# Performance work log

Measured on AMD Instinct MI355X. Metric: run time of the kernel, lower is better.

## Reference

```python
import jax, jax.numpy as jnp
import numpy as np

EPS = 1e-12  # F.normalize eps


def setup_inputs() -> dict:
    key = jax.random.key(0)
    k1, k2 = jax.random.split(key)
    B, T, C, E = 4, 4096, 2048, 64
    return {
        "hidden_states": jax.random.normal(k1, (B, T, C), dtype=jnp.float32),
        "sim_matrix": jax.random.normal(k2, (C, E), dtype=jnp.float32),
        "gates": jnp.zeros((E,), dtype=jnp.float32),
        "min_experts": 2,
    }


def reference(hidden_states, sim_matrix, gates, min_experts):
    b, t, c = hidden_states.shape
    h = hidden_states.reshape(b * t, c)
    # L2-normalize tokens (dim=-1) and expert columns (dim=0)
    hn = h / jnp.maximum(jnp.linalg.norm(h, axis=-1, keepdims=True), EPS)
    wn = sim_matrix / jnp.maximum(jnp.linalg.norm(sim_matrix, axis=0, keepdims=True), EPS)
    logits = hn @ wn - jax.nn.sigmoid(gates)          # [N, E]
    gated = jax.nn.relu(logits)
    # STE threshold (forward: hard 0/1 indicator)
    ind = (gated > 0).astype(gated.dtype)
    mask = gated + jax.lax.stop_gradient(ind - gated)
    # fallback: rows with no active expert get top-min_experts of raw logits
    inactive = jnp.sum(ind, axis=1) == 0              # [N]
    _, topk_idx = jax.lax.top_k(logits, min_experts)  # [N, k]
    n = mask.shape[0]
    fallback = jnp.zeros((n, logits.shape[1]), dtype=bool).at[
        jnp.arange(n)[:, None], topk_idx].set(True)
    put = inactive[:, None] & fallback                # positions overwritten with 1.0
    mask = jnp.where(put, jnp.asarray(1.0, mask.dtype), mask)
    masked = jnp.where(mask > 0, gated, -jnp.inf)
    routing_weights = jax.nn.softmax(masked, axis=-1)
    return routing_weights, logits, mask
```

## Files before the change

### kernel.cpp

```cpp
#include <hip/hip_runtime.h>
#include <math.h>

#define CDIM 2048
#define EDIM 64
#define BM   32
#define WSEG 512
#define NITW 8
#define PREPB 8

#define SCALE_H 1024.0f
#define SCALE_W 4096.0f
#define INV_SCALE (1.0f / 4194304.0f)

typedef float    f32x16 __attribute__((ext_vector_type(16)));
typedef float    f32x4v __attribute__((ext_vector_type(4)));
typedef _Float16 f16x8  __attribute__((ext_vector_type(8)));
typedef __fp16   cvt_t  __attribute__((ext_vector_type(2)));

__global__ void prep_w(const float* __restrict__ W,
                       unsigned short* __restrict__ bfrag,
                       float* __restrict__ pnw) {
    __shared__ float tile[256][65];
    __shared__ float part[4][64];
    const int t = threadIdx.x;
    const int c0 = blockIdx.x * 256;
#pragma unroll
    for (int p = 0; p < 16; ++p) {
        int r = (t >> 4) + p * 16;
        float4 v = *reinterpret_cast<const float4*>(W + (size_t)(c0 + r) * EDIM + (t & 15) * 4);
        tile[r][(t & 15) * 4 + 0] = v.x;
        tile[r][(t & 15) * 4 + 1] = v.y;
        tile[r][(t & 15) * 4 + 2] = v.z;
        tile[r][(t & 15) * 4 + 3] = v.w;
    }
    __syncthreads();
    {
        int g = t >> 6, e = t & 63;
        float s = 0.f;
#pragma unroll
        for (int j = 0; j < 64; ++j) { float v = tile[g * 64 + j][e]; s += v * v; }
        part[g][e] = s;
    }
    __syncthreads();
    if (t < 64) pnw[blockIdx.x * EDIM + t] = part[0][t] + part[1][t] + part[2][t] + part[3][t];

    const int nt = t >> 7, hl = (t >> 6) & 1, lane = t & 63;
    const int e = nt * 32 + (lane & 31);
    const int kb = (lane >> 5) * 8;
#pragma unroll
    for (int s = 0; s < 16; ++s) {
        int kl = s * 16 + kb;
        unsigned int wds[4];
#pragma unroll
        for (int pj = 0; pj < 4; ++pj) {
            float v0 = tile[kl + 2 * pj][e] * SCALE_W;
            float v1 = tile[kl + 2 * pj + 1][e] * SCALE_W;
            cvt_t hh = __builtin_amdgcn_cvt_pkrtz(v0, v1);
            if (hl) {
                cvt_t ll = __builtin_amdgcn_cvt_pkrtz(v0 - (float)hh[0], v1 - (float)hh[1]);
                wds[pj] = __builtin_bit_cast(unsigned int, ll);
            } else {
                wds[pj] = __builtin_bit_cast(unsigned int, hh);
            }
        }
        size_t off = ((size_t)(blockIdx.x * 16 + s)) * 2048 + (size_t)nt * 1024 + (size_t)hl * 512 + (size_t)lane * 8;
        *reinterpret_cast<uint4*>(bfrag + off) = make_uint4(wds[0], wds[1], wds[2], wds[3]);
    }
}

__launch_bounds__(256, 2)
__global__ void gating_main(const float* __restrict__ H,
                            const unsigned short* __restrict__ bfrag,
                            const float* __restrict__ pnw,
                            const float* __restrict__ gates,
                            float* __restrict__ out_rw,
                            float* __restrict__ out_lg,
                            float* __restrict__ out_mk) {
    __shared__ float aS[4][32][64];
    __shared__ float red[4][32][68];
    __shared__ float normred[4][32];
    __shared__ float invw_s[64];
    __shared__ float sig_s[64];

    const int t = threadIdx.x;
    const int w = t >> 6;
    const int l = t & 63;
    const int row0 = blockIdx.x * BM;
    const int kg = l >> 5;
    const int arow = l & 31;
    const int srow4 = l >> 4;
    const int sch = l & 15;

    if (t < 64) {
        float s2 = 0.f;
#pragma unroll
        for (int b = 0; b < PREPB; ++b) s2 += pnw[b * EDIM + t];
        invw_s[t] = 1.f / fmaxf(sqrtf(s2), 1e-12f);
        sig_s[t] = 1.f / (1.f + __expf(-gates[t]));
    }

    f32x16 acc[2][3];
#pragma unroll
    for (int a = 0; a < 2; ++a)
#pragma unroll
        for (int b = 0; b < 3; ++b)
#pragma unroll
            for (int i = 0; i < 16; ++i) acc[a][b][i] = 0.f;
    float nacc = 0.f;

#define STAGE1(J, IT) { \
    const int row_ = 4 * (J) + srow4; \
    const float* src_ = H + (size_t)(row0 + row_) * CDIM + w * WSEG + (IT) * 64 + ((sch ^ (row_ & 7)) << 2); \
    __builtin_amdgcn_global_load_lds((const __attribute__((address_space(1))) unsigned int*)src_, \
                                     (__attribute__((address_space(3))) unsigned int*)&aS[w][4 * (J)][0], 16, 0, 0); }
#define STAGE(IT) { STAGE1(0, IT); STAGE1(1, IT); STAGE1(2, IT); STAGE1(3, IT); \
                    STAGE1(4, IT); STAGE1(5, IT); STAGE1(6, IT); STAGE1(7, IT); }

    STAGE(0);
#pragma unroll
    for (int it = 0; it < NITW; ++it) {
        asm volatile("s_waitcnt vmcnt(0)" ::: "memory");
        __builtin_amdgcn_sched_barrier(0);
        f32x4v fr[8];
#pragma unroll
        for (int j = 0; j < 4; ++j) {
            int ca = (4 * j + 2 * kg) ^ (arow & 7);
            int cb = (4 * j + 2 * kg + 1) ^ (arow & 7);
            fr[2 * j]     = *reinterpret_cast<const f32x4v*>(&aS[w][arow][ca * 4]);
            fr[2 * j + 1] = *reinterpret_cast<const f32x4v*>(&aS[w][arow][cb * 4]);
        }
        asm volatile("s_waitcnt lgkmcnt(0)" ::: "memory");
        __builtin_amdgcn_sched_barrier(0);
        if (it + 1 < NITW) STAGE(it + 1);

#pragma unroll
        for (int j = 0; j < 4; ++j) {
            float f0 = fr[2*j][0], f1 = fr[2*j][1], f2 = fr[2*j][2], f3 = fr[2*j][3];
            float f4 = fr[2*j+1][0], f5 = fr[2*j+1][1], f6 = fr[2*j+1][2], f7 = fr[2*j+1][3];
            nacc += f0*f0 + f1*f1 + f2*f2 + f3*f3 + f4*f4 + f5*f5 + f6*f6 + f7*f7;
            float s0 = f0*SCALE_H, s1 = f1*SCALE_H, s2 = f2*SCALE_H, s3 = f3*SCALE_H;
            float s4 = f4*SCALE_H, s5 = f5*SCALE_H, s6 = f6*SCALE_H, s7 = f7*SCALE_H;
            cvt_t h0 = __builtin_amdgcn_cvt_pkrtz(s0, s1);
            cvt_t h1 = __builtin_amdgcn_cvt_pkrtz(s2, s3);
            cvt_t h2 = __builtin_amdgcn_cvt_pkrtz(s4, s5);
            cvt_t h3 = __builtin_amdgcn_cvt_pkrtz(s6, s7);
            cvt_t l0 = __builtin_amdgcn_cvt_pkrtz(s0 - (float)h0[0], s1 - (float)h0[1]);
            cvt_t l1 = __builtin_amdgcn_cvt_pkrtz(s2 - (float)h1[0], s3 - (float)h1[1]);
            cvt_t l2 = __builtin_amdgcn_cvt_pkrtz(s4 - (float)h2[0], s5 - (float)h2[1]);
            cvt_t l3 = __builtin_amdgcn_cvt_pkrtz(s6 - (float)h3[0], s7 - (float)h3[1]);
            f16x8 ah = __builtin_bit_cast(f16x8, make_uint4(
                __builtin_bit_cast(unsigned int, h0), __builtin_bit_cast(unsigned int, h1),
                __builtin_bit_cast(unsigned int, h2), __builtin_bit_cast(unsigned int, h3)));
            f16x8 al = __builtin_bit_cast(f16x8, make_uint4(
                __builtin_bit_cast(unsigned int, l0), __builtin_bit_cast(unsigned int, l1),
                __builtin_bit_cast(unsigned int, l2), __builtin_bit_cast(unsigned int, l3)));

            const unsigned short* bb = bfrag + ((size_t)(w * 32 + it * 4 + j)) * 2048 + (size_t)l * 8;
            f16x8 bh0 = __builtin_bit_cast(f16x8, *reinterpret_cast<const uint4*>(bb));
            f16x8 bl0 = __builtin_bit_cast(f16x8, *reinterpret_cast<const uint4*>(bb + 512));
            f16x8 bh1 = __builtin_bit_cast(f16x8, *reinterpret_cast<const uint4*>(bb + 1024));
            f16x8 bl1 = __builtin_bit_cast(f16x8, *reinterpret_cast<const uint4*>(bb + 1536));

            acc[0][0] = __builtin_amdgcn_mfma_f32_32x32x16_f16(ah, bh0, acc[0][0], 0, 0, 0);
            acc[0][1] = __builtin_amdgcn_mfma_f32_32x32x16_f16(ah, bl0, acc[0][1], 0, 0, 0);
            acc[0][2] = __builtin_amdgcn_mfma_f32_32x32x16_f16(al, bh0, acc[0][2], 0, 0, 0);
            acc[1][0] = __builtin_amdgcn_mfma_f32_32x32x16_f16(ah, bh1, acc[1][0], 0, 0, 0);
            acc[1][1] = __builtin_amdgcn_mfma_f32_32x32x16_f16(ah, bl1, acc[1][1], 0, 0, 0);
            acc[1][2] = __builtin_amdgcn_mfma_f32_32x32x16_f16(al, bh1, acc[1][2], 0, 0, 0);
        }
    }

#pragma unroll
    for (int nt = 0; nt < 2; ++nt)
#pragma unroll
        for (int r = 0; r < 16; ++r) {
            int rowl = (r & 3) + 8 * (r >> 2) + 4 * kg;
            red[w][rowl][nt * 32 + arow] = acc[nt][0][r] + acc[nt][1][r] + acc[nt][2][r];
        }
    nacc += __shfl_xor(nacc, 32);
    if (l < 32) normred[w][l] = nacc;
    __syncthreads();

    const int rr = t >> 3, e0 = (t & 7) * 8;
    const int orow = row0 + rr;
    float nh = normred[0][rr] + normred[1][rr] + normred[2][rr] + normred[3][rr];
    float invh = INV_SCALE / fmaxf(sqrtf(nh), 1e-12f);
    float lg[8];
#pragma unroll
    for (int k2 = 0; k2 < 8; ++k2) {
        int e = e0 + k2;
        float s = red[0][rr][e] + red[1][rr][e] + red[2][rr][e] + red[3][rr][e];
        lg[k2] = s * invh * invw_s[e] - sig_s[e];
    }
    float* plg = out_lg + (size_t)orow * EDIM + e0;
    *reinterpret_cast<float4*>(plg)     = make_float4(lg[0], lg[1], lg[2], lg[3]);
    *reinterpret_cast<float4*>(plg + 4) = make_float4(lg[4], lg[5], lg[6], lg[7]);

    float v1 = -INFINITY, v2 = -INFINITY;
    int i1 = 0x7fffffff, i2 = 0x7fffffff, cnt = 0;
#pragma unroll
    for (int j = 0; j < 8; ++j) {
        int e = e0 + j;
        float v = lg[j];
        cnt += (v > 0.f) ? 1 : 0;
        if (v > v1) { v2 = v1; i2 = i1; v1 = v; i1 = e; }
        else if (v > v2) { v2 = v; i2 = e; }
    }
#pragma unroll
    for (int st = 1; st <= 4; st <<= 1) {
        float w1 = __shfl_xor(v1, st);
        int   j1 = __shfl_xor(i1, st);
        float wv2 = __shfl_xor(v2, st);
        int   j2 = __shfl_xor(i2, st);
        int   cc = __shfl_xor(cnt, st);
        cnt += cc;
        bool g = (w1 > v1) || (w1 == v1 && j1 < i1);
        if (g) {
            bool g2 = (v1 > wv2) || (v1 == wv2 && i1 < j2);
            float nv2 = g2 ? v1 : wv2;
            int   ni2 = g2 ? i1 : j2;
            v1 = w1; i1 = j1; v2 = nv2; i2 = ni2;
        } else {
            bool g2 = (w1 > v2) || (w1 == v2 && j1 < i2);
            if (g2) { v2 = w1; i2 = j1; }
        }
    }
    bool act = cnt > 0;
    float rmax = act ? v1 : 0.f;
    float xs[8], ms[8];
    float wsum = 0.f;
#pragma unroll
    for (int j = 0; j < 8; ++j) {
        int e = e0 + j;
        float lv = lg[j];
        float x, m;
        if (act) {
            bool sel = lv > 0.f;
            m = sel ? 1.f : 0.f;
            x = sel ? __expf(lv - rmax) : 0.f;
        } else {
            bool sel = (e == i1) || (e == i2);
            m = sel ? 1.f : 0.f;
            x = m;
        }
        xs[j] = x; ms[j] = m; wsum += x;
    }
    wsum += __shfl_xor(wsum, 1);
    wsum += __shfl_xor(wsum, 2);
    wsum += __shfl_xor(wsum, 4);
    float invd = 1.f / wsum;
    float* prw = out_rw + (size_t)orow * EDIM + e0;
    float* pmk = out_mk + (size_t)orow * EDIM + e0;
    *reinterpret_cast<float4*>(prw)     = make_float4(xs[0]*invd, xs[1]*invd, xs[2]*invd, xs[3]*invd);
    *reinterpret_cast<float4*>(prw + 4) = make_float4(xs[4]*invd, xs[5]*invd, xs[6]*invd, xs[7]*invd);
    *reinterpret_cast<float4*>(pmk)     = make_float4(ms[0], ms[1], ms[2], ms[3]);
    *reinterpret_cast<float4*>(pmk + 4) = make_float4(ms[4], ms[5], ms[6], ms[7]);
}

extern "C" void kernel_launch(void* const* d_in, const int* in_sizes, int n_in,
                              void* d_out, int out_size, void* d_ws, size_t ws_size,
                              hipStream_t stream) {
    const float* H     = (const float*)d_in[0];
    const float* Wm    = (const float*)d_in[1];
    const float* gates = (const float*)d_in[2];
    const int ntok = in_sizes[0] / CDIM;

    unsigned short* bfrag = (unsigned short*)d_ws;
    float* pnw = (float*)(bfrag + (size_t)128 * 2048);

    float* out_rw = (float*)d_out;
    float* out_lg = out_rw + (size_t)ntok * EDIM;
    float* out_mk = out_lg + (size_t)ntok * EDIM;

    hipLaunchKernelGGL(prep_w, dim3(PREPB), dim3(256), 0, stream, Wm, bfrag, pnw);
    hipLaunchKernelGGL(gating_main, dim3(ntok / BM), dim3(256), 0, stream,
                       H, bfrag, pnw, gates, out_rw, out_lg, out_mk);
}
```

Before: 38.56 us.

## Split gating GEMM warps over K halves and expert halves with LDS double buffering

After: 40.81 us. +5.8%, slower.

```diff
diff --git a/kernel.cpp b/kernel.cpp
--- a/kernel.cpp
+++ b/kernel.cpp
@@ -4,9 +4,8 @@
 #define CDIM 2048
 #define EDIM 64
 #define BM   32
-#define WSEG 512
-#define NITW 8
-#define PREPB 8
+#define NIT  32
+#define PREPB 32
 
 #define SCALE_H 1024.0f
 #define SCALE_W 4096.0f
@@ -20,12 +19,12 @@
 __global__ void prep_w(const float* __restrict__ W,
                        unsigned short* __restrict__ bfrag,
                        float* __restrict__ pnw) {
-    __shared__ float tile[256][65];
+    __shared__ float tile[64][65];
     __shared__ float part[4][64];
     const int t = threadIdx.x;
-    const int c0 = blockIdx.x * 256;
-#pragma unroll
-    for (int p = 0; p < 16; ++p) {
+    const int c0 = blockIdx.x * 64;
+#pragma unroll
+    for (int p = 0; p < 4; ++p) {
         int r = (t >> 4) + p * 16;
         float4 v = *reinterpret_cast<const float4*>(W + (size_t)(c0 + r) * EDIM + (t & 15) * 4);
         tile[r][(t & 15) * 4 + 0] = v.x;
@@ -38,17 +37,16 @@
         int g = t >> 6, e = t & 63;
         float s = 0.f;
 #pragma unroll
-        for (int j = 0; j < 64; ++j) { float v = tile[g * 64 + j][e]; s += v * v; }
+        for (int j = 0; j < 16; ++j) { float v = tile[g * 16 + j][e]; s += v * v; }
         part[g][e] = s;
     }
     __syncthreads();
     if (t < 64) pnw[blockIdx.x * EDIM + t] = part[0][t] + part[1][t] + part[2][t] + part[3][t];
-
     const int nt = t >> 7, hl = (t >> 6) & 1, lane = t & 63;
     const int e = nt * 32 + (lane & 31);
     const int kb = (lane >> 5) * 8;
 #pragma unroll
-    for (int s = 0; s < 16; ++s) {
+    for (int s = 0; s < 4; ++s) {
         int kl = s * 16 + kb;
         unsigned int wds[4];
 #pragma unroll
@@ -63,9 +61,90 @@
                 wds[pj] = __builtin_bit_cast(unsigned int, hh);
             }
         }
-        size_t off = ((size_t)(blockIdx.x * 16 + s)) * 2048 + (size_t)nt * 1024 + (size_t)hl * 512 + (size_t)lane * 8;
+        size_t off = ((size_t)(blockIdx.x * 4 + s)) * 2048 + (size_t)nt * 1024 + (size_t)hl * 512 + (size_t)lane * 8;
         *reinterpret_cast<uint4*>(bfrag + off) = make_uint4(wds[0], wds[1], wds[2], wds[3]);
     }
+}
+
+template<int BUF>
+__device__ __forceinline__ void stage_it(
+    int it, int e, int ks, int w, int l, int row0,
+    const float* __restrict__ H, const unsigned short* __restrict__ bfrag,
+    float (&aS)[2][2][32][32], unsigned short (&bS)[4][2][4][512])
+{
+    if (e == 0) {
+#pragma unroll
+        for (int J = 0; J < 4; ++J) {
+            const float* srcA = H + (size_t)(row0 + 8 * J + (l >> 3)) * CDIM
+                              + ks * 1024 + it * 32 + (((l & 7) ^ (l >> 3)) << 2);
+            __builtin_amdgcn_global_load_lds(
+                (const __attribute__((address_space(1))) unsigned int*)srcA,
+                (__attribute__((address_space(3))) unsigned int*)&aS[ks][BUF][8 * J][0], 16, 0, 0);
+        }
+    }
+#pragma unroll
+    for (int m = 0; m < 4; ++m) {
+        const unsigned short* srcB = bfrag + (size_t)(ks * 64 + it * 2 + (m >> 1)) * 2048
+                                   + (size_t)e * 1024 + (size_t)(m & 1) * 512 + (size_t)l * 8;
+        __builtin_amdgcn_global_load_lds(
+            (const __attribute__((address_space(1))) unsigned int*)srcB,
+            (__attribute__((address_space(3))) unsigned int*)&bS[w][BUF][m][0], 16, 0, 0);
+    }
+}
+
+template<int CUR, int STG>
+__device__ __forceinline__ void kstep(
+    int it, int e, int ks, int w, int l, int row0,
+    const float* __restrict__ H, const unsigned short* __restrict__ bfrag,
+    float (&aS)[2][2][32][32], unsigned short (&bS)[4][2][4][512],
+    f32x16* acc, float& nacc)
+{
+    if (STG) stage_it<CUR ^ 1>(it + 1, e, ks, w, l, row0, H, bfrag, aS, bS);
+    if (STG) {
+        if (e == 0) { asm volatile("s_waitcnt vmcnt(8)" ::: "memory"); }
+        else        { asm volatile("s_waitcnt vmcnt(4)" ::: "memory"); }
+    } else {
+        asm volatile("s_waitcnt vmcnt(0)" ::: "memory");
+    }
+    __builtin_amdgcn_sched_barrier(0);
+    __builtin_amdgcn_s_barrier();
+    __builtin_amdgcn_sched_barrier(0);
+
+    const int r = l & 31, kg = l >> 5;
+#pragma unroll
+    for (int j = 0; j < 2; ++j) {
+        const f32x4v a0 = *reinterpret_cast<const f32x4v*>(
+            &aS[ks][CUR][r][((4 * j + 2 * kg + 0) ^ (r & 7)) * 4]);
+        const f32x4v a1 = *reinterpret_cast<const f32x4v*>(
+            &aS[ks][CUR][r][((4 * j + 2 * kg + 1) ^ (r & 7)) * 4]);
+        float f0 = a0[0], f1 = a0[1], f2 = a0[2], f3 = a0[3];
+        float f4 = a1[0], f5 = a1[1], f6 = a1[2], f7 = a1[3];
+        nacc += f0*f0 + f1*f1 + f2*f2 + f3*f3 + f4*f4 + f5*f5 + f6*f6 + f7*f7;
+        float s0 = f0*SCALE_H, s1 = f1*SCALE_H, s2 = f2*SCALE_H, s3 = f3*SCALE_H;
+        float s4 = f4*SCALE_H, s5 = f5*SCALE_H, s6 = f6*SCALE_H, s7 = f7*SCALE_H;
+        cvt_t h0 = __builtin_amdgcn_cvt_pkrtz(s0, s1);
+        cvt_t h1 = __builtin_amdgcn_cvt_pkrtz(s2, s3);
+        cvt_t h2 = __builtin_amdgcn_cvt_pkrtz(s4, s5);
+        cvt_t h3 = __builtin_amdgcn_cvt_pkrtz(s6, s7);
+        cvt_t l0 = __builtin_amdgcn_cvt_pkrtz(s0 - (float)h0[0], s1 - (float)h0[1]);
+        cvt_t l1 = __builtin_amdgcn_cvt_pkrtz(s2 - (float)h1[0], s3 - (float)h1[1]);
+        cvt_t l2 = __builtin_amdgcn_cvt_pkrtz(s4 - (float)h2[0], s5 - (float)h2[1]);
+        cvt_t l3 = __builtin_amdgcn_cvt_pkrtz(s6 - (float)h3[0], s7 - (float)h3[1]);
+        f16x8 ah = __builtin_bit_cast(f16x8, make_uint4(
+            __builtin_bit_cast(unsigned int, h0), __builtin_bit_cast(unsigned int, h1),
+            __builtin_bit_cast(unsigned int, h2), __builtin_bit_cast(unsigned int, h3)));
+        f16x8 al = __builtin_bit_cast(f16x8, make_uint4(
+            __builtin_bit_cast(unsigned int, l0), __builtin_bit_cast(unsigned int, l1),
+            __builtin_bit_cast(unsigned int, l2), __builtin_bit_cast(unsigned int, l3)));
+        f16x8 bh = *reinterpret_cast<const f16x8*>(&bS[w][CUR][2 * j + 0][l * 8]);
+        f16x8 bl = *reinterpret_cast<const f16x8*>(&bS[w][CUR][2 * j + 1][l * 8]);
+        acc[0] = __builtin_amdgcn_mfma_f32_32x32x16_f16(ah, bh, acc[0], 0, 0, 0);
+        acc[1] = __builtin_amdgcn_mfma_f32_32x32x16_f16(ah, bl, acc[1], 0, 0, 0);
+        acc[2] = __builtin_amdgcn_mfma_f32_32x32x16_f16(al, bh, acc[2], 0, 0, 0);
+    }
+    __builtin_amdgcn_sched_barrier(0);
+    __builtin_amdgcn_s_barrier();
+    __builtin_amdgcn_sched_barrier(0);
 }
 
 __launch_bounds__(256, 2)
@@ -76,20 +155,18 @@
                             float* __restrict__ out_rw,
                             float* __restrict__ out_lg,
                             float* __restrict__ out_mk) {
-    __shared__ float aS[4][32][64];
-    __shared__ float red[4][32][68];
-    __shared__ float normred[4][32];
+    __shared__ float aS[2][2][32][32];
+    __shared__ unsigned short bS[4][2][4][512];
+    __shared__ float red[2][32][36];
+    __shared__ float normred[2][32];
     __shared__ float invw_s[64];
     __shared__ float sig_s[64];
 
     const int t = threadIdx.x;
-    const int w = t >> 6;
-    const int l = t & 63;
+    const int w = t >> 6, l = t & 63;
+    const int e = w & 1, ks = w >> 1;
     const int row0 = blockIdx.x * BM;
-    const int kg = l >> 5;
-    const int arow = l & 31;
-    const int srow4 = l >> 4;
-    const int sch = l & 15;
+    const int kg = l >> 5, arow = l & 31;
 
     if (t < 64) {
         float s2 = 0.f;
@@ -98,99 +175,52 @@
         invw_s[t] = 1.f / fmaxf(sqrtf(s2), 1e-12f);
         sig_s[t] = 1.f / (1.f + __expf(-gates[t]));
     }
-
-    f32x16 acc[2][3];
-#pragma unroll
-    for (int a = 0; a < 2; ++a)
-#pragma unroll
-        for (int b = 0; b < 3; ++b)
-#pragma unroll
-            for (int i = 0; i < 16; ++i) acc[a][b][i] = 0.f;
+    __builtin_amdgcn_sched_barrier(0);
+
+    f32x16 acc[3];
+#pragma unroll
+    for (int b = 0; b < 3; ++b)
+#pragma unroll
+        for (int i = 0; i < 16; ++i) acc[b][i] = 0.f;
     float nacc = 0.f;
 
-#define STAGE1(J, IT) { \
-    const int row_ = 4 * (J) + srow4; \
-    const float* src_ = H + (size_t)(row0 + row_) * CDIM + w * WSEG + (IT) * 64 + ((sch ^ (row_ & 7)) << 2); \
-    __builtin_amdgcn_global_load_lds((const __attribute__((address_space(1))) unsigned int*)src_, \
-                                     (__attribute__((address_space(3))) unsigned int*)&aS[w][4 * (J)][0], 16, 0, 0); }
-#define STAGE(IT) { STAGE1(0, IT); STAGE1(1, IT); STAGE1(2, IT); STAGE1(3, IT); \
-                    STAGE1(4, IT); STAGE1(5, IT); STAGE1(6, IT); STAGE1(7, IT); }
-
-    STAGE(0);
-#pragma unroll
-    for (int it = 0; it < NITW; ++it) {
-        asm volatile("s_waitcnt vmcnt(0)" ::: "memory");
-        __builtin_amdgcn_sched_barrier(0);
-        f32x4v fr[8];
-#pragma unroll
-        for (int j = 0; j < 4; ++j) {
-            int ca = (4 * j + 2 * kg) ^ (arow & 7);
-            int cb = (4 * j + 2 * kg + 1) ^ (arow & 7);
-            fr[2 * j]     = *reinterpret_cast<const f32x4v*>(&aS[w][arow][ca * 4]);
-            fr[2 * j + 1] = *reinterpret_cast<const f32x4v*>(&aS[w][arow][cb * 4]);
-        }
-        asm volatile("s_waitcnt lgkmcnt(0)" ::: "memory");
-        __builtin_amdgcn_sched_barrier(0);
-        if (it + 1 < NITW) STAGE(it + 1);
-
-#pragma unroll
-        for (int j = 0; j < 4; ++j) {
-            float f0 = fr[2*j][0], f1 = fr[2*j][1], f2 = fr[2*j][2], f3 = fr[2*j][3];
-            float f4 = fr[2*j+1][0], f5 = fr[2*j+1][1], f6 = fr[2*j+1][2], f7 = fr[2*j+1][3];
-            nacc += f0*f0 + f1*f1 + f2*f2 + f3*f3 + f4*f4 + f5*f5 + f6*f6 + f7*f7;
-            float s0 = f0*SCALE_H, s1 = f1*SCALE_H, s2 = f2*SCALE_H, s3 = f3*SCALE_H;
-            float s4 = f4*SCALE_H, s5 = f5*SCALE_H, s6 = f6*SCALE_H, s7 = f7*SCALE_H;
-            cvt_t h0 = __builtin_amdgcn_cvt_pkrtz(s0, s1);
-            cvt_t h1 = __builtin_amdgcn_cvt_pkrtz(s2, s3);
-            cvt_t h2 = __builtin_amdgcn_cvt_pkrtz(s4, s5);
-            cvt_t h3 = __builtin_amdgcn_cvt_pkrtz(s6, s7);
-            cvt_t l0 = __builtin_amdgcn_cvt_pkrtz(s0 - (float)h0[0], s1 - (float)h0[1]);
-            cvt_t l1 = __builtin_amdgcn_cvt_pkrtz(s2 - (float)h1[0], s3 - (float)h1[1]);
-            cvt_t l2 = __builtin_amdgcn_cvt_pkrtz(s4 - (float)h2[0], s5 - (float)h2[1]);
-            cvt_t l3 = __builtin_amdgcn_cvt_pkrtz(s6 - (float)h3[0], s7 - (float)h3[1]);
-            f16x8 ah = __builtin_bit_cast(f16x8, make_uint4(
-                __builtin_bit_cast(unsigned int, h0), __builtin_bit_cast(unsigned int, h1),
-                __builtin_bit_cast(unsigned int, h2), __builtin_bit_cast(unsigned int, h3)));
-            f16x8 al = __builtin_bit_cast(f16x8, make_uint4(
-                __builtin_bit_cast(unsigned int, l0), __builtin_bit_cast(unsigned int, l1),
-                __builtin_bit_cast(unsigned int, l2), __builtin_bit_cast(unsigned int, l3)));
-
-            const unsigned short* bb = bfrag + ((size_t)(w * 32 + it * 4 + j)) * 2048 + (size_t)l * 8;
-            f16x8 bh0 = __builtin_bit_cast(f16x8, *reinterpret_cast<const uint4*>(bb));
-            f16x8 bl0 = __builtin_bit_cast(f16x8, *reinterpret_cast<const uint4*>(bb + 512));
-            f16x8 bh1 = __builtin_bit_cast(f16x8, *reinterpret_cast<const uint4*>(bb + 1024));
-            f16x8 bl1 = __builtin_bit_cast(f16x8, *reinterpret_cast<const uint4*>(bb + 1536));
-
-            acc[0][0] = __builtin_amdgcn_mfma_f32_32x32x16_f16(ah, bh0, acc[0][0], 0, 0, 0);
-            acc[0][1] = __builtin_amdgcn_mfma_f32_32x32x16_f16(ah, bl0, acc[0][1], 0, 0, 0);
-            acc[0][2] = __builtin_amdgcn_mfma_f32_32x32x16_f16(al, bh0, acc[0][2], 0, 0, 0);
-            acc[1][0] = __builtin_amdgcn_mfma_f32_32x32x16_f16(ah, bh1, acc[1][0], 0, 0, 0);
-            acc[1][1] = __builtin_amdgcn_mfma_f32_32x32x16_f16(ah, bl1, acc[1][1], 0, 0, 0);
-            acc[1][2] = __builtin_amdgcn_mfma_f32_32x32x16_f16(al, bh1, acc[1][2], 0, 0, 0);
-        }
-    }
-
-#pragma unroll
-    for (int nt = 0; nt < 2; ++nt)
+    stage_it<0>(0, e, ks, w, l, row0, H, bfrag, aS, bS);
+    for (int ot = 0; ot < 15; ++ot) {
+        kstep<0, 1>(2 * ot,     e, ks, w, l, row0, H, bfrag, aS, bS, acc, nacc);
+        kstep<1, 1>(2 * ot + 1, e, ks, w, l, row0, H, bfrag, aS, bS, acc, nacc);
+    }
+    kstep<0, 1>(30, e, ks, w, l, row0, H, bfrag, aS, bS, acc, nacc);
+    kstep<1, 0>(31, e, ks, w, l, row0, H, bfrag, aS, bS, acc, nacc);
+
+    nacc += __shfl_xor(nacc, 32);
+    if (e == 0 && l < 32) normred[ks][l] = nacc;
+    if (ks == 0) {
 #pragma unroll
         for (int r = 0; r < 16; ++r) {
             int rowl = (r & 3) + 8 * (r >> 2) + 4 * kg;
-            red[w][rowl][nt * 32 + arow] = acc[nt][0][r] + acc[nt][1][r] + acc[nt][2][r];
-        }
-    nacc += __shfl_xor(nacc, 32);
-    if (l < 32) normred[w][l] = nacc;
+            red[e][rowl][arow] = acc[0][r] + acc[1][r] + acc[2][r];
+        }
+    }
+    __syncthreads();
+    if (ks == 1) {
+#pragma unroll
+        for (int r = 0; r < 16; ++r) {
+            int rowl = (r & 3) + 8 * (r >> 2) + 4 * kg;
+            red[e][rowl][arow] += acc[0][r] + acc[1][r] + acc[2][r];
+        }
+    }
     __syncthreads();
 
     const int rr = t >> 3, e0 = (t & 7) * 8;
     const int orow = row0 + rr;
-    float nh = normred[0][rr] + normred[1][rr] + normred[2][rr] + normred[3][rr];
+    const int eh = e0 >> 5, ec = e0 & 31;
+    float nh = normred[0][rr] + normred[1][rr];
     float invh = INV_SCALE / fmaxf(sqrtf(nh), 1e-12f);
     float lg[8];
 #pragma unroll
     for (int k2 = 0; k2 < 8; ++k2) {
-        int e = e0 + k2;
-        float s = red[0][rr][e] + red[1][rr][e] + red[2][rr][e] + red[3][rr][e];
-        lg[k2] = s * invh * invw_s[e] - sig_s[e];
+        int ee = e0 + k2;
+        lg[k2] = red[eh][rr][ec + k2] * invh * invw_s[ee] - sig_s[ee];
     }
     float* plg = out_lg + (size_t)orow * EDIM + e0;
     *reinterpret_cast<float4*>(plg)     = make_float4(lg[0], lg[1], lg[2], lg[3]);
@@ -200,11 +230,11 @@
     int i1 = 0x7fffffff, i2 = 0x7fffffff, cnt = 0;
 #pragma unroll
     for (int j = 0; j < 8; ++j) {
-        int e = e0 + j;
+        int ee = e0 + j;
         float v = lg[j];
         cnt += (v > 0.f) ? 1 : 0;
-        if (v > v1) { v2 = v1; i2 = i1; v1 = v; i1 = e; }
-        else if (v > v2) { v2 = v; i2 = e; }
+        if (v > v1) { v2 = v1; i2 = i1; v1 = v; i1 = ee; }
+        else if (v > v2) { v2 = v; i2 = ee; }
     }
 #pragma unroll
     for (int st = 1; st <= 4; st <<= 1) {
@@ -231,7 +261,7 @@
     float wsum = 0.f;
 #pragma unroll
     for (int j = 0; j < 8; ++j) {
-        int e = e0 + j;
+        int ee = e0 + j;
         float lv = lg[j];
         float x, m;
         if (act) {
@@ -239,7 +269,7 @@
             m = sel ? 1.f : 0.f;
             x = sel ? __expf(lv - rmax) : 0.f;
         } else {
-            bool sel = (e == i1) || (e == i2);
+            bool sel = (ee == i1) || (ee == i2);
             m = sel ? 1.f : 0.f;
             x = m;
         }
```
